# Performance work log

Measured on AMD Instinct MI355X. Metric: run time of the kernel, lower is better.

The kernel has to match this reference:

```python
import jax, jax.numpy as jnp
import numpy as np

NEG_INF = -1e30  # used via float('-inf') in original; -inf literal is fine too


def setup_inputs() -> dict:
    key = jax.random.key(0)
    kq, kk, kv = jax.random.split(key, 3)
    b, h, s, d = 2, 32, 2048, 128
    q = jax.random.normal(kq, (b, h, s, d), dtype=jnp.float32)
    k = jax.random.normal(kk, (b, h, s, d), dtype=jnp.float32)
    v = jax.random.normal(kv, (b, h, s, d), dtype=jnp.float32)
    # causal mask, True = masked (matches the module's `~tril` path when mask is None)
    mask = ~jnp.tril(jnp.ones((s, s), dtype=bool))
    attention_mask = jnp.broadcast_to(mask[None, None], (b, 1, s, s))
    return {"query_layer": q, "key_layer": k, "value_layer": v,
            "attention_mask": attention_mask}


def reference(query_layer, key_layer, value_layer, attention_mask):
    b, h, sq, hd = query_layer.shape
    norm_factor = jnp.sqrt(jnp.asarray(hd, dtype=query_layer.dtype))
    # scores: [b, h, sq, sk], computed in fp32 as in the original (.float())
    scores = jnp.einsum('bhqd,bhkd->bhqk', query_layer, key_layer) / norm_factor
    scores = scores.astype(jnp.float32)
    scores = jnp.where(attention_mask, -jnp.inf, scores)
    probs = jax.nn.softmax(scores, axis=-1).astype(value_layer.dtype)
    # context: [b, h, sq, hd]
    ctx = jnp.einsum('bhqk,bhkd->bhqd', probs, value_layer)
    # -> [b, sq, h*hd]
    ctx = jnp.transpose(ctx, (0, 2, 1, 3)).reshape(b, sq, h * hd)
    return ctx
```

## Files before the change

### kernel.cpp

```cpp
#include <hip/hip_runtime.h>
#include <hip/hip_bf16.h>

typedef __attribute__((ext_vector_type(8))) short bf16x8;
typedef __attribute__((ext_vector_type(8))) unsigned short u16x8;
typedef __attribute__((ext_vector_type(4))) float f32x4;

#define S_LEN 2048
#define D_DIM 128
#define BH_NUM 64
#define OUT_W 4096

__device__ __forceinline__ unsigned short f2bf(float f){
  unsigned int u = __float_as_uint(f);
  u += 0x7FFFu + ((u >> 16) & 1u);
  return (unsigned short)(u >> 16);
}

__device__ __forceinline__ short pbf(float f){
  __hip_bfloat16 h = __float2bfloat16(f);
  return *reinterpret_cast<short*>(&h);
}

__device__ __forceinline__ void gl_lds16(const void* g, void* l){
  __builtin_amdgcn_global_load_lds(
      (const __attribute__((address_space(1))) unsigned int*)g,
      (__attribute__((address_space(3))) unsigned int*)l, 16, 0, 0);
}

__global__ __launch_bounds__(256) void conv_bf16(const float* __restrict__ in,
                                                 unsigned short* __restrict__ out, int n8){
  int i = blockIdx.x * 256 + threadIdx.x;
  if (i < n8){
    const float4* p = (const float4*)(in + (size_t)i * 8);
    float4 a = p[0], b = p[1];
    u16x8 o;
    o[0]=f2bf(a.x); o[1]=f2bf(a.y); o[2]=f2bf(a.z); o[3]=f2bf(a.w);
    o[4]=f2bf(b.x); o[5]=f2bf(b.y); o[6]=f2bf(b.z); o[7]=f2bf(b.w);
    *(u16x8*)(out + (size_t)i * 8) = o;
  }
}

__global__ __launch_bounds__(256) void conv_vt(const float* __restrict__ V,
                                               unsigned short* __restrict__ Vt){
  __shared__ unsigned short lt[256][36];
  const int t = threadIdx.x;
  const int key0 = blockIdx.x * 256;
  const int d0   = blockIdx.y * 32;
  const int bh   = blockIdx.z;
  const float* src = V + ((size_t)bh * S_LEN + key0 + t) * D_DIM + d0;
  #pragma unroll
  for (int j = 0; j < 8; ++j){
    float4 v = *(const float4*)(src + j * 4);
    ushort4 pk; pk.x=f2bf(v.x); pk.y=f2bf(v.y); pk.z=f2bf(v.z); pk.w=f2bf(v.w);
    *(ushort4*)&lt[t][j * 4] = pk;
  }
  __syncthreads();
  #pragma unroll
  for (int uu = 0; uu < 4; ++uu){
    int u  = uu * 256 + t;
    int d  = u >> 5;
    int j8 = u & 31;
    int b64 = j8 >> 3, m8 = j8 & 7;
    int ks2 = m8 >> 2, t4m = m8 & 3;
    u16x8 o;
    #pragma unroll
    for (int i = 0; i < 8; ++i){
      int srck = b64 * 64 + ks2 * 32 + (i >> 2) * 16 + t4m * 4 + (i & 3);
      o[i] = lt[srck][d];
    }
    *(u16x8*)(Vt + ((size_t)bh * D_DIM + d0 + d) * S_LEN + key0 + j8 * 8) = o;
  }
}

__device__ __forceinline__ void tile_compute(
    const unsigned short* __restrict__ kb, const unsigned short* __restrict__ vb,
    const bf16x8 (&qf0)[4], const bf16x8 (&qf1)[4],
    f32x4 (&o0)[8], f32x4 (&o1)[8],
    float& l0, float& l1,
    int kvb, int qw0, int qw1, int c, int t4)
{
  const int cx = c & 7;
  f32x4 s0[2], s1[2];
  #pragma unroll
  for (int g = 0; g < 2; ++g){ s0[g] = (f32x4){0,0,0,0}; s1[g] = (f32x4){0,0,0,0}; }
  __builtin_amdgcn_s_setprio(1);
  #pragma unroll
  for (int g = 0; g < 2; ++g){
    const unsigned short* krow = kb + (size_t)(g * 16 + c) * D_DIM;
    #pragma unroll
    for (int ks = 0; ks < 4; ++ks){
      bf16x8 kf = *(const bf16x8*)(krow + (((ks * 4 + t4) ^ cx) * 8));
      s0[g] = __builtin_amdgcn_mfma_f32_16x16x32_bf16(kf, qf0[ks], s0[g], 0, 0, 0);
      s1[g] = __builtin_amdgcn_mfma_f32_16x16x32_bf16(kf, qf1[ks], s1[g], 0, 0, 0);
    }
  }
  __builtin_amdgcn_s_setprio(0);
  if (kvb + 31 > qw0){
    int q = qw0 + c;
    #pragma unroll
    for (int g = 0; g < 2; ++g)
      #pragma unroll
      for (int r = 0; r < 4; ++r)
        if (kvb + g * 16 + t4 * 4 + r > q) s0[g][r] = -1e30f;
  }
  if (kvb + 31 > qw1){
    int q = qw1 + c;
    #pragma unroll
    for (int g = 0; g < 2; ++g)
      #pragma unroll
      for (int r = 0; r < 4; ++r)
        if (kvb + g * 16 + t4 * 4 + r > q) s1[g][r] = -1e30f;
  }
  bf16x8 p0, p1;
  #pragma unroll
  for (int g = 0; g < 2; ++g)
    #pragma unroll
    for (int r = 0; r < 4; ++r){
      float e0 = exp2f(s0[g][r]); l0 += e0; p0[g*4+r] = pbf(e0);
      float e1 = exp2f(s1[g][r]); l1 += e1; p1[g*4+r] = pbf(e1);
    }
  __builtin_amdgcn_s_setprio(1);
  #pragma unroll
  for (int db = 0; db < 8; ++db){
    const unsigned short* vrow = vb + (size_t)(db * 16 + c) * 32;
    bf16x8 vf = *(const bf16x8*)(vrow + ((t4 ^ (c & 3)) * 8));
    o0[db] = __builtin_amdgcn_mfma_f32_16x16x32_bf16(p0, vf, o0[db], 0, 0, 0);
    o1[db] = __builtin_amdgcn_mfma_f32_16x16x32_bf16(p1, vf, o1[db], 0, 0, 0);
  }
  __builtin_amdgcn_s_setprio(0);
}

__global__ __launch_bounds__(256, 3) void attn_fwd_bf16(
    const float* __restrict__ Qg, const unsigned short* __restrict__ Kw,
    const unsigned short* __restrict__ Vw, float* __restrict__ Og)
{
  __shared__ unsigned short Kl[2][32 * 128];
  __shared__ unsigned short Vl[2][128 * 32];

  const int tid  = threadIdx.x;
  const int lane = tid & 63;
  const int w    = tid >> 6;
  const int c    = lane & 15;
  const int t4   = lane >> 4;
  const int bh   = blockIdx.x;
  const int tq   = 15 - blockIdx.y;
  const unsigned short* Kbh = Kw + (size_t)bh * S_LEN * D_DIM;
  const unsigned short* Vbh = Vw + (size_t)bh * S_LEN * D_DIM;
  const float* Qbh = Qg + (size_t)bh * S_LEN * D_DIM;
  const int bi = bh >> 5, hh = bh & 31;
  const float QS = 0.12751743f;

  const int q0  = tq * 128;
  const int qw0 = q0 + 32 * w;
  const int qw1 = qw0 + 16;

  bf16x8 qf0[4], qf1[4];
  {
    const float* r0 = Qbh + (size_t)(qw0 + c) * D_DIM + t4 * 8;
    const float* r1 = Qbh + (size_t)(qw1 + c) * D_DIM + t4 * 8;
    #pragma unroll
    for (int ks = 0; ks < 4; ++ks){
      float4 a = *(const float4*)(r0 + ks * 32);
      float4 b = *(const float4*)(r0 + ks * 32 + 4);
      bf16x8 f;
      f[0]=pbf(a.x*QS); f[1]=pbf(a.y*QS); f[2]=pbf(a.z*QS); f[3]=pbf(a.w*QS);
      f[4]=pbf(b.x*QS); f[5]=pbf(b.y*QS); f[6]=pbf(b.z*QS); f[7]=pbf(b.w*QS);
      qf0[ks] = f;
      a = *(const float4*)(r1 + ks * 32);
      b = *(const float4*)(r1 + ks * 32 + 4);
      f[0]=pbf(a.x*QS); f[1]=pbf(a.y*QS); f[2]=pbf(a.z*QS); f[3]=pbf(a.w*QS);
      f[4]=pbf(b.x*QS); f[5]=pbf(b.y*QS); f[6]=pbf(b.z*QS); f[7]=pbf(b.w*QS);
      qf1[ks] = f;
    }
  }

  f32x4 o0[8], o1[8];
  #pragma unroll
  for (int db = 0; db < 8; ++db){ o0[db] = (f32x4){0,0,0,0}; o1[db] = (f32x4){0,0,0,0}; }
  float l0 = 0.f, l1 = 0.f;

  const int ch1 = tid + 256;
  const unsigned short* ks0 = Kbh + (size_t)(tid >> 4) * D_DIM + (((tid & 15) ^ ((tid >> 4) & 7)) * 8);
  const unsigned short* ks1 = Kbh + (size_t)(ch1 >> 4) * D_DIM + (((ch1 & 15) ^ ((ch1 >> 4) & 7)) * 8);
  const unsigned short* vs0 = Vbh + (size_t)(tid >> 2) * S_LEN + (((tid & 3) ^ ((tid >> 2) & 3)) * 8);
  const unsigned short* vs1 = Vbh + (size_t)(ch1 >> 2) * S_LEN + (((ch1 & 3) ^ ((ch1 >> 2) & 3)) * 8);
  const int du0 = w * 512;
  const int du1 = 2048 + w * 512;

  #define STAGE(KB, VB) do { \
      gl_lds16(ks0, (KB) + du0); gl_lds16(ks1, (KB) + du1); \
      gl_lds16(vs0, (VB) + du0); gl_lds16(vs1, (VB) + du1); \
      ks0 += 32 * D_DIM; ks1 += 32 * D_DIM; vs0 += 32; vs1 += 32; } while(0)

  const int nt   = 4 * tq + 4;
  const int kmax = qw0 + 31;

  STAGE(Kl[0], Vl[0]);
  for (int it = 0; it < nt; it += 2){
    __syncthreads();
    STAGE(Kl[1], Vl[1]);
    if (it * 32 <= kmax)
      tile_compute(Kl[0], Vl[0], qf0, qf1, o0, o1, l0, l1,
                   it * 32, qw0, qw1, c, t4);
    __syncthreads();
    if (it + 2 < nt)
      STAGE(Kl[0], Vl[0]);
    if ((it + 1) * 32 <= kmax)
      tile_compute(Kl[1], Vl[1], qf0, qf1, o0, o1, l0, l1,
                   (it + 1) * 32, qw0, qw1, c, t4);
  }
  #undef STAGE

  l0 += __shfl_xor(l0, 16); l0 += __shfl_xor(l0, 32);
  l1 += __shfl_xor(l1, 16); l1 += __shfl_xor(l1, 32);
  float* ob0 = Og + ((size_t)bi * S_LEN + qw0) * OUT_W + hh * D_DIM;
  float* ob1 = Og + ((size_t)bi * S_LEN + qw1) * OUT_W + hh * D_DIM;
  #pragma unroll
  for (int r = 0; r < 4; ++r){
    float lr0 = __shfl(l0, t4 * 4 + r), lr1 = __shfl(l1, t4 * 4 + r);
    float i0 = 1.0f / lr0, i1 = 1.0f / lr1;
    float* w0 = ob0 + (size_t)(t4 * 4 + r) * OUT_W;
    float* w1 = ob1 + (size_t)(t4 * 4 + r) * OUT_W;
    #pragma unroll
    for (int db = 0; db < 8; ++db){
      w0[db * 16 + c] = o0[db][r] * i0;
      w1[db * 16 + c] = o1[db][r] * i1;
    }
  }
}

__global__ __launch_bounds__(256) void attn_fwd(
    const float* __restrict__ Qg, const float* __restrict__ Kg,
    const float* __restrict__ Vg, float* __restrict__ Og)
{
  __shared__ unsigned short Kfb[32][136];
  __shared__ unsigned short Vfb[128][40];
  const int tid  = threadIdx.x;
  const int lane = tid & 63;
  const int w    = tid >> 6;
  const int c    = lane & 15;
  const int t4   = lane >> 4;
  const int q0 = blockIdx.x * 64;
  const int bh = blockIdx.y;
  const size_t base = (size_t)bh * S_LEN * D_DIM;
  const float* Qp = Qg + base;
  const float* Kp = Kg + base;
  const float* Vp = Vg + base;
  const int qw = q0 + w * 16;
  const float QSCALE = 0.08838834764831845f;
  bf16x8 qf[4];
  {
    const float* qrow = Qp + (size_t)(qw + c) * D_DIM + t4 * 8;
    #pragma unroll
    for (int ks = 0; ks < 4; ++ks){
      float4 a = *(const float4*)(qrow + ks * 32);
      float4 b = *(const float4*)(qrow + ks * 32 + 4);
      bf16x8 f;
      f[0]=(short)f2bf(a.x*QSCALE); f[1]=(short)f2bf(a.y*QSCALE);
      f[2]=(short)f2bf(a.z*QSCALE); f[3]=(short)f2bf(a.w*QSCALE);
      f[4]=(short)f2bf(b.x*QSCALE); f[5]=(short)f2bf(b.y*QSCALE);
      f[6]=(short)f2bf(b.z*QSCALE); f[7]=(short)f2bf(b.w*QSCALE);
      qf[ks] = f;
    }
  }
  f32x4 o[8];
  #pragma unroll
  for (int db = 0; db < 8; ++db) o[db] = (f32x4){0.f,0.f,0.f,0.f};
  float m_run = -1e30f, l_run = 0.f;
  const int ntiles = q0 / 32 + 2;
  for (int it = 0; it < ntiles; ++it){
    const int kvb = it * 32;
    #pragma unroll
    for (int rr = 0; rr < 4; ++rr){
      int f   = rr * 256 + tid;
      int key = f >> 5;
      int d0  = (f & 31) * 4;
      float4 k4 = *(const float4*)(Kp + (size_t)(kvb + key) * D_DIM + d0);
      ushort4 pk;
      pk.x = f2bf(k4.x); pk.y = f2bf(k4.y); pk.z = f2bf(k4.z); pk.w = f2bf(k4.w);
      *(ushort4*)&Kfb[key][d0] = pk;
      float4 v4 = *(const float4*)(Vp + (size_t)(kvb + key) * D_DIM + d0);
      int kp = ((key & 15) >> 2) * 8 + (key >> 4) * 4 + (key & 3);
      Vfb[d0 + 0][kp] = f2bf(v4.x);
      Vfb[d0 + 1][kp] = f2bf(v4.y);
      Vfb[d0 + 2][kp] = f2bf(v4.z);
      Vfb[d0 + 3][kp] = f2bf(v4.w);
    }
    __syncthreads();
    if (kvb <= qw + 15){
      f32x4 sg[2];
      #pragma unroll
      for (int g = 0; g < 2; ++g){
        f32x4 acc = (f32x4){0.f,0.f,0.f,0.f};
        #pragma unroll
        for (int ks = 0; ks < 4; ++ks){
          bf16x8 kf = *(const bf16x8*)&Kfb[g*16 + c][ks*32 + t4*8];
          acc = __builtin_amdgcn_mfma_f32_16x16x32_bf16(kf, qf[ks], acc, 0, 0, 0);
        }
        sg[g] = acc;
      }
      if (kvb + 31 > qw){
        int q = qw + c;
        #pragma unroll
        for (int g = 0; g < 2; ++g)
          #pragma unroll
          for (int r = 0; r < 4; ++r){
            int key = kvb + g*16 + t4*4 + r;
            if (key > q) sg[g][r] = -1e30f;
          }
      }
      float mt = sg[0][0];
      #pragma unroll
      for (int g = 0; g < 2; ++g)
        #pragma unroll
        for (int r = 0; r < 4; ++r) mt = fmaxf(mt, sg[g][r]);
      mt = fmaxf(mt, __shfl_xor(mt, 16));
      mt = fmaxf(mt, __shfl_xor(mt, 32));
      float m_new = fmaxf(m_run, mt);
      float alpha = __expf(m_run - m_new);
      m_run = m_new;
      float p[8];
      float rs = 0.f;
      #pragma unroll
      for (int i = 0; i < 8; ++i){
        p[i] = __expf(sg[i>>2][i&3] - m_new);
        rs += p[i];
      }
      rs += __shfl_xor(rs, 16);
      rs += __shfl_xor(rs, 32);
      l_run = l_run * alpha + rs;
      bf16x8 pf;
      #pragma unroll
      for (int i = 0; i < 8; ++i) pf[i] = (short)f2bf(p[i]);
      float a_out[4];
      #pragma unroll
      for (int r = 0; r < 4; ++r) a_out[r] = __shfl(alpha, t4*4 + r);
      #pragma unroll
      for (int db = 0; db < 8; ++db){
        #pragma unroll
        for (int r = 0; r < 4; ++r) o[db][r] *= a_out[r];
      }
      #pragma unroll
      for (int db = 0; db < 8; ++db){
        bf16x8 vf = *(const bf16x8*)&Vfb[db*16 + c][t4*8];
        o[db] = __builtin_amdgcn_mfma_f32_16x16x32_bf16(pf, vf, o[db], 0, 0, 0);
      }
    }
    __syncthreads();
  }
  const int bi = bh >> 5;
  const int hfb = bh & 31;
  float* obase = Og + ((size_t)bi * S_LEN + qw) * OUT_W + hfb * D_DIM;
  #pragma unroll
  for (int r = 0; r < 4; ++r){
    float lrr = __shfl(l_run, t4*4 + r);
    float inv = 1.0f / lrr;
    float* orow = obase + (size_t)(t4*4 + r) * OUT_W;
    #pragma unroll
    for (int db = 0; db < 8; ++db)
      orow[db*16 + c] = o[db][r] * inv;
  }
}

extern "C" void kernel_launch(void* const* d_in, const int* in_sizes, int n_in,
                              void* d_out, int out_size, void* d_ws, size_t ws_size,
                              hipStream_t stream)
{
  const float* Q = (const float*)d_in[0];
  const float* K = (const float*)d_in[1];
  const float* V = (const float*)d_in[2];
  float* O = (float*)d_out;
  const size_t elems = (size_t)BH_NUM * S_LEN * D_DIM;
  const size_t need  = elems * 2 * 2;
  if (ws_size >= need){
    unsigned short* Kw = (unsigned short*)d_ws;
    unsigned short* Vt = Kw + elems;
    conv_bf16<<<(int)(elems / 8 / 256), 256, 0, stream>>>(K, Kw, (int)(elems / 8));
    conv_vt<<<dim3(S_LEN / 256, D_DIM / 32, BH_NUM), 256, 0, stream>>>(V, Vt);
    attn_fwd_bf16<<<dim3(BH_NUM, 16), 256, 0, stream>>>(Q, Kw, Vt, O);
  } else {
    attn_fwd<<<dim3(S_LEN / 64, BH_NUM), 256, 0, stream>>>(Q, K, V, O);
  }
}
```

Measured before the change: 139.9 us.

## Halve query tile per block to 64 rows, one 16-row group per wave

Each block now handles 64 query rows instead of 128, with each wave computing a single 16-row query group instead of two, so the grid doubles to 32 query tiles per head and launch bounds allow 4 blocks per CU. This cuts per-thread registers (one accumulator set) and improves load balance across the causal triangle, raising occupancy. The cost is that each K/V tile staged into LDS is reused by half as many query rows, which doubles global/LDS traffic for K and V per unit of compute.

After: 150.7 us. 1.08x slower.

```diff
diff --git a/kernel.cpp b/kernel.cpp
--- a/kernel.cpp
+++ b/kernel.cpp
@@ -74,15 +74,12 @@
 
 __device__ __forceinline__ void tile_compute(
     const unsigned short* __restrict__ kb, const unsigned short* __restrict__ vb,
-    const bf16x8 (&qf0)[4], const bf16x8 (&qf1)[4],
-    f32x4 (&o0)[8], f32x4 (&o1)[8],
-    float& l0, float& l1,
-    int kvb, int qw0, int qw1, int c, int t4)
+    const bf16x8 (&qf)[4], f32x4 (&o)[8], float& l,
+    int kvb, int qw, int c, int t4)
 {
   const int cx = c & 7;
-  f32x4 s0[2], s1[2];
-  #pragma unroll
-  for (int g = 0; g < 2; ++g){ s0[g] = (f32x4){0,0,0,0}; s1[g] = (f32x4){0,0,0,0}; }
+  f32x4 s[2];
+  s[0] = (f32x4){0,0,0,0}; s[1] = (f32x4){0,0,0,0};
   __builtin_amdgcn_s_setprio(1);
   #pragma unroll
   for (int g = 0; g < 2; ++g){
@@ -90,47 +87,36 @@
     #pragma unroll
     for (int ks = 0; ks < 4; ++ks){
       bf16x8 kf = *(const bf16x8*)(krow + (((ks * 4 + t4) ^ cx) * 8));
-      s0[g] = __builtin_amdgcn_mfma_f32_16x16x32_bf16(kf, qf0[ks], s0[g], 0, 0, 0);
-      s1[g] = __builtin_amdgcn_mfma_f32_16x16x32_bf16(kf, qf1[ks], s1[g], 0, 0, 0);
+      s[g] = __builtin_amdgcn_mfma_f32_16x16x32_bf16(kf, qf[ks], s[g], 0, 0, 0);
     }
   }
   __builtin_amdgcn_s_setprio(0);
-  if (kvb + 31 > qw0){
-    int q = qw0 + c;
+  if (kvb + 31 > qw){
+    int q = qw + c;
     #pragma unroll
     for (int g = 0; g < 2; ++g)
       #pragma unroll
       for (int r = 0; r < 4; ++r)
-        if (kvb + g * 16 + t4 * 4 + r > q) s0[g][r] = -1e30f;
-  }
-  if (kvb + 31 > qw1){
-    int q = qw1 + c;
-    #pragma unroll
-    for (int g = 0; g < 2; ++g)
-      #pragma unroll
-      for (int r = 0; r < 4; ++r)
-        if (kvb + g * 16 + t4 * 4 + r > q) s1[g][r] = -1e30f;
-  }
-  bf16x8 p0, p1;
+        if (kvb + g * 16 + t4 * 4 + r > q) s[g][r] = -1e30f;
+  }
+  bf16x8 p;
   #pragma unroll
   for (int g = 0; g < 2; ++g)
     #pragma unroll
     for (int r = 0; r < 4; ++r){
-      float e0 = exp2f(s0[g][r]); l0 += e0; p0[g*4+r] = pbf(e0);
-      float e1 = exp2f(s1[g][r]); l1 += e1; p1[g*4+r] = pbf(e1);
+      float e = exp2f(s[g][r]); l += e; p[g*4+r] = pbf(e);
     }
   __builtin_amdgcn_s_setprio(1);
   #pragma unroll
   for (int db = 0; db < 8; ++db){
     const unsigned short* vrow = vb + (size_t)(db * 16 + c) * 32;
     bf16x8 vf = *(const bf16x8*)(vrow + ((t4 ^ (c & 3)) * 8));
-    o0[db] = __builtin_amdgcn_mfma_f32_16x16x32_bf16(p0, vf, o0[db], 0, 0, 0);
-    o1[db] = __builtin_amdgcn_mfma_f32_16x16x32_bf16(p1, vf, o1[db], 0, 0, 0);
+    o[db] = __builtin_amdgcn_mfma_f32_16x16x32_bf16(p, vf, o[db], 0, 0, 0);
   }
   __builtin_amdgcn_s_setprio(0);
 }
 
-__global__ __launch_bounds__(256, 3) void attn_fwd_bf16(
+__global__ __launch_bounds__(256, 4) void attn_fwd_bf16(
     const float* __restrict__ Qg, const unsigned short* __restrict__ Kw,
     const unsigned short* __restrict__ Vw, float* __restrict__ Og)
 {
@@ -143,21 +129,19 @@
   const int c    = lane & 15;
   const int t4   = lane >> 4;
   const int bh   = blockIdx.x;
-  const int tq   = 15 - blockIdx.y;
+  const int tq   = 31 - blockIdx.y;
   const unsigned short* Kbh = Kw + (size_t)bh * S_LEN * D_DIM;
   const unsigned short* Vbh = Vw + (size_t)bh * S_LEN * D_DIM;
   const float* Qbh = Qg + (size_t)bh * S_LEN * D_DIM;
   const int bi = bh >> 5, hh = bh & 31;
   const float QS = 0.12751743f;
 
-  const int q0  = tq * 128;
-  const int qw0 = q0 + 32 * w;
-  const int qw1 = qw0 + 16;
-
-  bf16x8 qf0[4], qf1[4];
+  const int q0 = tq * 64;
+  const int qw = q0 + 16 * w;
+
+  bf16x8 qf[4];
   {
-    const float* r0 = Qbh + (size_t)(qw0 + c) * D_DIM + t4 * 8;
-    const float* r1 = Qbh + (size_t)(qw1 + c) * D_DIM + t4 * 8;
+    const float* r0 = Qbh + (size_t)(qw + c) * D_DIM + t4 * 8;
     #pragma unroll
     for (int ks = 0; ks < 4; ++ks){
       float4 a = *(const float4*)(r0 + ks * 32);
@@ -165,19 +149,14 @@
       bf16x8 f;
       f[0]=pbf(a.x*QS); f[1]=pbf(a.y*QS); f[2]=pbf(a.z*QS); f[3]=pbf(a.w*QS);
       f[4]=pbf(b.x*QS); f[5]=pbf(b.y*QS); f[6]=pbf(b.z*QS); f[7]=pbf(b.w*QS);
-      qf0[ks] = f;
-      a = *(const float4*)(r1 + ks * 32);
-      b = *(const float4*)(r1 + ks * 32 + 4);
-      f[0]=pbf(a.x*QS); f[1]=pbf(a.y*QS); f[2]=pbf(a.z*QS); f[3]=pbf(a.w*QS);
-      f[4]=pbf(b.x*QS); f[5]=pbf(b.y*QS); f[6]=pbf(b.z*QS); f[7]=pbf(b.w*QS);
-      qf1[ks] = f;
-    }
-  }
-
-  f32x4 o0[8], o1[8];
-  #pragma unroll
-  for (int db = 0; db < 8; ++db){ o0[db] = (f32x4){0,0,0,0}; o1[db] = (f32x4){0,0,0,0}; }
-  float l0 = 0.f, l1 = 0.f;
+      qf[ks] = f;
+    }
+  }
+
+  f32x4 o[8];
+  #pragma unroll
+  for (int db = 0; db < 8; ++db) o[db] = (f32x4){0,0,0,0};
+  float l = 0.f;
 
   const int ch1 = tid + 256;
   const unsigned short* ks0 = Kbh + (size_t)(tid >> 4) * D_DIM + (((tid & 15) ^ ((tid >> 4) & 7)) * 8);
@@ -192,40 +171,33 @@
       gl_lds16(vs0, (VB) + du0); gl_lds16(vs1, (VB) + du1); \
       ks0 += 32 * D_DIM; ks1 += 32 * D_DIM; vs0 += 32; vs1 += 32; } while(0)
 
-  const int nt   = 4 * tq + 4;
-  const int kmax = qw0 + 31;
+  const int nt   = 2 * tq + 2;
+  const int kmax = qw + 15;
 
   STAGE(Kl[0], Vl[0]);
   for (int it = 0; it < nt; it += 2){
     __syncthreads();
     STAGE(Kl[1], Vl[1]);
     if (it * 32 <= kmax)
-      tile_compute(Kl[0], Vl[0], qf0, qf1, o0, o1, l0, l1,
-                   it * 32, qw0, qw1, c, t4);
+      tile_compute(Kl[0], Vl[0], qf, o, l, it * 32, qw, c, t4);
     __syncthreads();
     if (it + 2 < nt)
       STAGE(Kl[0], Vl[0]);
     if ((it + 1) * 32 <= kmax)
-      tile_compute(Kl[1], Vl[1], qf0, qf1, o0, o1, l0, l1,
-                   (it + 1) * 32, qw0, qw1, c, t4);
+      tile_compute(Kl[1], Vl[1], qf, o, l, (it + 1) * 32, qw, c, t4);
   }
   #undef STAGE
 
-  l0 += __shfl_xor(l0, 16); l0 += __shfl_xor(l0, 32);
-  l1 += __shfl_xor(l1, 16); l1 += __shfl_xor(l1, 32);
-  float* ob0 = Og + ((size_t)bi * S_LEN + qw0) * OUT_W + hh * D_DIM;
-  float* ob1 = Og + ((size_t)bi * S_LEN + qw1) * OUT_W + hh * D_DIM;
+  l += __shfl_xor(l, 16); l += __shfl_xor(l, 32);
+  float* ob = Og + ((size_t)bi * S_LEN + qw) * OUT_W + hh * D_DIM;
   #pragma unroll
   for (int r = 0; r < 4; ++r){
-    float lr0 = __shfl(l0, t4 * 4 + r), lr1 = __shfl(l1, t4 * 4 + r);
-    float i0 = 1.0f / lr0, i1 = 1.0f / lr1;
-    float* w0 = ob0 + (size_t)(t4 * 4 + r) * OUT_W;
-    float* w1 = ob1 + (size_t)(t4 * 4 + r) * OUT_W;
-    #pragma unroll
-    for (int db = 0; db < 8; ++db){
-      w0[db * 16 + c] = o0[db][r] * i0;
-      w1[db * 16 + c] = o1[db][r] * i1;
-    }
+    float lr = __shfl(l, t4 * 4 + r);
+    float iv = 1.0f / lr;
+    float* w0 = ob + (size_t)(t4 * 4 + r) * OUT_W;
+    #pragma unroll
+    for (int db = 0; db < 8; ++db)
+      w0[db * 16 + c] = o[db][r] * iv;
   }
 }
 
@@ -377,7 +349,7 @@
     unsigned short* Vt = Kw + elems;
     conv_bf16<<<(int)(elems / 8 / 256), 256, 0, stream>>>(K, Kw, (int)(elems / 8));
     conv_vt<<<dim3(S_LEN / 256, D_DIM / 32, BH_NUM), 256, 0, stream>>>(V, Vt);
-    attn_fwd_bf16<<<dim3(BH_NUM, 16), 256, 0, stream>>>(Q, Kw, Vt, O);
+    attn_fwd_bf16<<<dim3(BH_NUM, 32), 256, 0, stream>>>(Q, Kw, Vt, O);
   } else {
     attn_fwd<<<dim3(S_LEN / 64, BH_NUM), 256, 0, stream>>>(Q, K, V, O);
   }
```
